# Performance work log

Measured on AMD Instinct MI355X. Metric: run time of the kernel, lower is better.

## Reference

```python
import jax, jax.numpy as jnp
import numpy as np

EPS = 1e-05
TEMP = 0.03


def setup_inputs() -> dict:
    key = jax.random.key(0)
    ks = jax.random.split(key, 5)
    bs, d = 256, 768
    code_vec = jax.random.normal(ks[0], (bs, d), dtype=jnp.float32)
    nl_vec = jax.random.normal(ks[1], (bs, d), dtype=jnp.float32)
    code_aug_vec = jax.random.normal(ks[2], (bs, d), dtype=jnp.float32)
    W1 = jax.random.normal(ks[3], (4 * d, d), dtype=jnp.float32) / np.sqrt(4 * d)
    b1 = jnp.zeros((d,), dtype=jnp.float32)
    W2 = jax.random.normal(ks[4], (d, 1), dtype=jnp.float32) / np.sqrt(d)
    b2 = jnp.zeros((1,), dtype=jnp.float32)
    return {"code_vec": code_vec, "nl_vec": nl_vec, "code_aug_vec": code_aug_vec,
            "W1": W1, "b1": b1, "W2": W2, "b2": b2}


def _pair_logits(nl, code, W1, b1, W2, b2):
    # MLP(cat([nl_i, code_j, nl_i - code_j, nl_i * code_j])) without the 4d concat:
    # split W1 rows into the four 768-blocks.
    d = nl.shape[1]
    Wa, Wb, Wc, Wd = W1[:d], W1[d:2 * d], W1[2 * d:3 * d], W1[3 * d:]
    lin = (nl @ (Wa + Wc))[:, None, :] + (code @ (Wb - Wc))[None, :, :]  # [bs,bs,768]
    prod = jnp.einsum('id,jd,dh->ijh', nl, code, Wd)                      # [bs,bs,768]
    h = jnp.tanh(lin + prod + b1)
    return jax.nn.sigmoid(jnp.einsum('ijh,ho->ij', h, W2) + b2[0])        # [bs,bs]


def _masked_softmax_loss(logits, mask):
    # -log((softmax(logits) * mask).sum(1))
    p = jax.nn.softmax(logits, axis=1)
    return -jnp.log((p * mask).sum(1))


def reference(code_vec, nl_vec, code_aug_vec, W1, b1, W2, b2):
    bs = code_vec.shape[0]
    eye = jnp.eye(bs, dtype=code_vec.dtype)

    # CE over dot-product scores with diagonal labels
    scores = nl_vec @ code_vec.T
    loss_ce = -jnp.mean(jnp.diagonal(jax.nn.log_softmax(scores, axis=1)))

    # Pairwise concat-MLP binary loss
    logits = _pair_logits(nl_vec, code_vec, W1, b1, W2, b2)
    poss = jnp.diagonal(logits)
    neg_log = jnp.log(1.0 - logits + EPS) * (1.0 - eye)
    negs_mean = neg_log.sum() / (bs * (bs - 1))
    loss_cls = -(negs_mean + jnp.mean(jnp.log(poss + EPS)))

    # InfoNCE-style multi-term contrastive loss
    cf = code_vec / jnp.linalg.norm(code_vec, axis=1, keepdims=True)
    nf = nl_vec / jnp.linalg.norm(nl_vec, axis=1, keepdims=True)
    af = code_aug_vec / jnp.linalg.norm(code_aug_vec, axis=1, keepdims=True)

    l_code_p = (cf @ nf.T) / TEMP
    l_nl_p = (nf @ cf.T) / TEMP
    l_code_n = ((cf @ cf.T) / TEMP) * (1.0 - eye)
    l_nl_n = ((nf @ nf.T) / TEMP) * (1.0 - eye)
    l_code_pa = (cf @ af.T) / TEMP
    l_nl_pa = (nf @ af.T) / TEMP

    code_logits = jnp.concatenate([l_code_p, 0.8 * l_code_n, 0.1 * l_code_pa], axis=1)
    nl_logits = jnp.concatenate([l_nl_p, 0.8 * l_nl_n, 0.1 * l_nl_pa], axis=1)
    zeros = jnp.zeros((bs, bs), dtype=code_vec.dtype)
    mask = jnp.concatenate([eye, zeros, eye], axis=1)

    loss_code = _masked_softmax_loss(code_logits, mask)
    loss_nl = _masked_softmax_loss(nl_logits, mask)
    loss_clr = (loss_code.mean() + loss_nl.mean()) / 2.0

    loss = loss_ce + 0.1 * loss_clr + loss_cls
    return (loss, code_vec, nl_vec)
```

## Files before the change

kernel.cpp:

```cpp
#include <hip/hip_runtime.h>
#include <stdint.h>

#define EPSV 1e-5f
#define INVT (1.0f/0.03f)

typedef _Float16 halfx8 __attribute__((ext_vector_type(8)));
typedef float f32x4 __attribute__((ext_vector_type(4)));

__device__ __forceinline__ unsigned short f2h(float f) {
  _Float16 h = (_Float16)f;
  return __builtin_bit_cast(unsigned short, h);
}

__device__ __forceinline__ float wave_sum(float v) {
  #pragma unroll
  for (int m = 32; m; m >>= 1) v += __shfl_xor(v, m);
  return v;
}
__device__ __forceinline__ float wave_max(float v) {
  #pragma unroll
  for (int m = 32; m; m >>= 1) v = fmaxf(v, __shfl_xor(v, m));
  return v;
}
__device__ __forceinline__ float block_sum(float v, float* sred) {
  v = wave_sum(v);
  __syncthreads();
  if ((threadIdx.x & 63) == 0) sred[threadIdx.x >> 6] = v;
  __syncthreads();
  return sred[0] + sred[1] + sred[2] + sred[3];
}
__device__ __forceinline__ float block_max(float v, float* sred) {
  v = wave_max(v);
  __syncthreads();
  if ((threadIdx.x & 63) == 0) sred[threadIdx.x >> 6] = v;
  __syncthreads();
  return fmaxf(fmaxf(sred[0], sred[1]), fmaxf(sred[2], sred[3]));
}

__device__ __forceinline__ void gload_lds16(const void* g, void* l) {
  __builtin_amdgcn_global_load_lds((__attribute__((address_space(1))) void*)g,
                                   (__attribute__((address_space(3))) void*)l, 16, 0, 0);
}

__global__ __launch_bounds__(256) void k_prep(
    const float* __restrict__ code, const float* __restrict__ nl, const float* __restrict__ aug,
    const float* __restrict__ W1,
    unsigned short* __restrict__ code_f16, unsigned short* __restrict__ nl_f16,
    unsigned short* __restrict__ WdT, unsigned short* __restrict__ WbcT,
    unsigned short* __restrict__ lin1_f16,
    float* __restrict__ invc, float* __restrict__ invn, float* __restrict__ inva,
    float* __restrict__ G,
    float* __restrict__ out, float* __restrict__ s_sum, float* __restrict__ accv) {
  __shared__ __align__(16) float smem[4112];
  const int b = blockIdx.x, tid = threadIdx.x;

  if (b < 96) {
    const int rt = b / 12, ct = b % 12;
    const int r0 = rt * 32, c0 = ct * 64;
    float* Xs = smem;
    float* Ws = smem + 1056;
    const int tx = tid & 15, ty = tid >> 4;
    float a[2][4] = {};
    for (int kt = 0; kt < 24; ++kt) {
      const int k0 = kt * 32;
      __syncthreads();
      #pragma unroll
      for (int q = 0; q < 4; ++q) {
        int e = q * 256 + tid;
        int row = e >> 5, k = e & 31;
        Xs[row * 33 + k] = nl[(r0 + row) * 768 + k0 + k];
      }
      #pragma unroll
      for (int q = 0; q < 8; ++q) {
        int e = q * 256 + tid;
        int k = e >> 6, c = e & 63;
        Ws[k * 64 + c] = W1[(k0 + k) * 768 + c0 + c] + W1[(1536 + k0 + k) * 768 + c0 + c];
      }
      __syncthreads();
      #pragma unroll
      for (int k = 0; k < 32; ++k) {
        float xa = Xs[ty * 33 + k], xb = Xs[(ty + 16) * 33 + k];
        float w0 = Ws[k * 64 + tx], w1 = Ws[k * 64 + tx + 16];
        float w2 = Ws[k * 64 + tx + 32], w3 = Ws[k * 64 + tx + 48];
        a[0][0] += xa * w0; a[0][1] += xa * w1; a[0][2] += xa * w2; a[0][3] += xa * w3;
        a[1][0] += xb * w0; a[1][1] += xb * w1; a[1][2] += xb * w2; a[1][3] += xb * w3;
      }
    }
    #pragma unroll
    for (int dy = 0; dy < 2; ++dy)
      #pragma unroll
      for (int m = 0; m < 4; ++m)
        lin1_f16[(r0 + ty + dy * 16) * 768 + c0 + tx + m * 16] = f2h(a[dy][m]);

  } else if (b < 416) {
    const int bb = b - 96;
    const int mat = bb >> 6;
    const int tile = bb & 63;
    const int y0 = (tile >> 3) * 32, x0 = (tile & 7) * 32;
    const float* X; const float* Y;
    if (mat == 0)      { X = nl;   Y = code; }
    else if (mat == 1) { X = code; Y = code; }
    else if (mat == 2) { X = nl;   Y = nl;   }
    else if (mat == 3) { X = code; Y = aug;  }
    else               { X = nl;   Y = aug;  }
    float* outg = G + mat * 65536;
    float* Xs = smem;
    float* Ys = smem + 2048;
    const int tx = tid & 15, ty = tid >> 4;
    float a00 = 0, a01 = 0, a10 = 0, a11 = 0;
    for (int kt = 0; kt < 12; ++kt) {
      const int k0 = kt * 64;
      __syncthreads();
      #pragma unroll
      for (int q = 0; q < 2; ++q) {
        int chunk = q * 256 + tid;
        int row = chunk >> 4, c4 = chunk & 15;
        float4 xv = *(const float4*)(X + (y0 + row) * 768 + k0 + c4 * 4);
        float4 yv = *(const float4*)(Y + (x0 + row) * 768 + k0 + c4 * 4);
        *(float4*)(Xs + row * 64 + ((c4 ^ (row & 15)) << 2)) = xv;
        *(float4*)(Ys + row * 64 + ((c4 ^ (row & 15)) << 2)) = yv;
      }
      __syncthreads();
      #pragma unroll
      for (int c4 = 0; c4 < 16; ++c4) {
        float4 xa = *(const float4*)(Xs + ty * 64 + ((c4 ^ ty) << 2));
        float4 xb = *(const float4*)(Xs + (ty + 16) * 64 + ((c4 ^ ty) << 2));
        float4 ya = *(const float4*)(Ys + tx * 64 + ((c4 ^ tx) << 2));
        float4 yb = *(const float4*)(Ys + (tx + 16) * 64 + ((c4 ^ tx) << 2));
        a00 += xa.x * ya.x + xa.y * ya.y + xa.z * ya.z + xa.w * ya.w;
        a01 += xa.x * yb.x + xa.y * yb.y + xa.z * yb.z + xa.w * yb.w;
        a10 += xb.x * ya.x + xb.y * ya.y + xb.z * ya.z + xb.w * ya.w;
        a11 += xb.x * yb.x + xb.y * yb.y + xb.z * yb.z + xb.w * yb.w;
      }
    }
    outg[(y0 + ty) * 256 + x0 + tx] = a00;
    outg[(y0 + ty) * 256 + x0 + tx + 16] = a01;
    outg[(y0 + ty + 16) * 256 + x0 + tx] = a10;
    outg[(y0 + ty + 16) * 256 + x0 + tx + 16] = a11;

  } else if (b < 800) {
    const int idx = (b - 416) * 256 + tid;
    if (idx < 49152) {
      float4 v = ((const float4*)code)[idx];
      ushort4 o; o.x = f2h(v.x); o.y = f2h(v.y); o.z = f2h(v.z); o.w = f2h(v.w);
      ((ushort4*)code_f16)[idx] = o;
    } else {
      const int q = idx - 49152;
      float4 v = ((const float4*)nl)[q];
      ushort4 o; o.x = f2h(v.x); o.y = f2h(v.y); o.z = f2h(v.z); o.w = f2h(v.w);
      ((ushort4*)nl_f16)[q] = o;
    }

  } else if (b < 1376) {
    float (*tile)[33] = (float(*)[33])smem;
    const int bb = b - 800;
    const int bx = bb % 24, by = bb / 24;
    const int tx = tid & 31, ty = tid >> 5;
    const int h0 = bx * 32, d0 = by * 32;
    #pragma unroll
    for (int yy = 0; yy < 4; ++yy) {
      int dd = ty + yy * 8;
      tile[dd][tx] = W1[(2304 + d0 + dd) * 768 + h0 + tx];
    }
    __syncthreads();
    #pragma unroll
    for (int yy = 0; yy < 4; ++yy) {
      int hh = ty + yy * 8;
      WdT[(h0 + hh) * 768 + d0 + tx] = f2h(tile[tx][hh]);
    }

  } else if (b < 1952) {
    float (*tile)[33] = (float(*)[33])smem;
    const int bb = b - 1376;
    const int bx = bb % 24, by = bb / 24;
    const int tx = tid & 31, ty = tid >> 5;
    const int h0 = bx * 32, d0 = by * 32;
    #pragma unroll
    for (int yy = 0; yy < 4; ++yy) {
      int dd = ty + yy * 8;
      tile[dd][tx] = W1[(768 + d0 + dd) * 768 + h0 + tx] - W1[(1536 + d0 + dd) * 768 + h0 + tx];
    }
    __syncthreads();
    #pragma unroll
    for (int yy = 0; yy < 4; ++yy) {
      int hh = ty + yy * 8;
      WbcT[(h0 + hh) * 768 + d0 + tx] = f2h(tile[tx][hh]);
    }

  } else if (b < 2144) {
    const int rr = (b - 1952) * 4 + (tid >> 6);
    const int mat = rr >> 8, row = rr & 255;
    const float* src = (mat == 0) ? code : (mat == 1) ? nl : aug;
    const int l = tid & 63;
    float s = 0.f;
    #pragma unroll
    for (int t = 0; t < 12; ++t) { float v = src[row * 768 + l + t * 64]; s += v * v; }
    s = wave_sum(s);
    if (l == 0) ((mat == 0) ? invc : (mat == 1) ? invn : inva)[row] = rsqrtf(s);

  } else if (b < 2528) {
    const int idx = (b - 2144) * 256 + tid;
    for (int t = idx; t < 196608; t += 384 * 256) {
      out[1 + t] = code[t];
      out[1 + 196608 + t] = nl[t];
    }

  } else {
    const int idx = (b - 2528) * 256 + tid;
    ((float4*)s_sum)[idx] = make_float4(0.f, 0.f, 0.f, 0.f);
    if (b == 2528 && tid < 16) accv[tid] = 0.f;
  }
}

__global__ __launch_bounds__(512, 4) void k_pair(
    const unsigned short* __restrict__ code_f16, const unsigned short* __restrict__ nl_f16,
    const unsigned short* __restrict__ WdT, const unsigned short* __restrict__ WbcT,
    const unsigned short* __restrict__ lin1_f16,
    const float* __restrict__ b1, const float* __restrict__ W2,
    float* __restrict__ s_sum) {
  __shared__ __align__(16) unsigned short Alds[256 * 64];
  __shared__ __align__(16) unsigned short Blds[128 * 64];
  __shared__ float linb[128];
  __shared__ float w2s[128];
  __shared__ float part[2][256];

  const int tid = threadIdx.x;
  const int bid = blockIdx.x;
  const int ct = bid >> 8;
  const int i  = bid & 255;
  const int h0 = ct << 7;

  if (tid < 128) {
    linb[tid] = (float)((const _Float16*)lin1_f16)[i * 768 + h0 + tid] + b1[h0 + tid];
    w2s[tid]  = W2[h0 + tid];
  }

  const int w = tid >> 6, lane = tid & 63;
  const int lr = lane & 15, g = lane >> 4;
  const int wr = (w >> 1) << 6;
  const int wcIdx = w & 1;
  const int wc = wcIdx << 6;
  const int c4 = tid & 7, rg = tid >> 3;

  f32x4 acc[4][4] = {};

  auto stage_A = [&](int kt) {
    const int k0 = kt << 6;
    #pragma unroll
    for (int q = 0; q < 4; ++q) {
      const int chunk = q * 512 + tid;
      const int row = chunk >> 3, c = chunk & 7;
      const unsigned short* src = code_f16 + row * 768 + k0 + ((c ^ (row & 7)) << 3);
      char* dst = (char*)Alds + (q * 512 + w * 64) * 16;
      gload_lds16(src, dst);
    }
  };

  auto stageB = [&](int kt) {
    const int k0 = kt << 6;
    const uint4 nv  = *(const uint4*)(nl_f16 + i * 768 + k0 + (c4 << 3));
    const uint4 wv0 = *(const uint4*)(WdT  + (h0 + rg) * 768 + k0 + (c4 << 3));
    const uint4 bv0 = *(const uint4*)(WbcT + (h0 + rg) * 768 + k0 + (c4 << 3));
    const uint4 wv1 = *(const uint4*)(WdT  + (h0 + rg + 64) * 768 + k0 + (c4 << 3));
    const uint4 bv1 = *(const uint4*)(WbcT + (h0 + rg + 64) * 768 + k0 + (c4 << 3));
    uint4 p0, p1;
    asm("v_pk_fma_f16 %0, %1, %2, %3" : "=v"(p0.x) : "v"(nv.x), "v"(wv0.x), "v"(bv0.x));
    asm("v_pk_fma_f16 %0, %1, %2, %3" : "=v"(p0.y) : "v"(nv.y), "v"(wv0.y), "v"(bv0.y));
    asm("v_pk_fma_f16 %0, %1, %2, %3" : "=v"(p0.z) : "v"(nv.z), "v"(wv0.z), "v"(bv0.z));
    asm("v_pk_fma_f16 %0, %1, %2, %3" : "=v"(p0.w) : "v"(nv.w), "v"(wv0.w), "v"(bv0.w));
    asm("v_pk_fma_f16 %0, %1, %2, %3" : "=v"(p1.x) : "v"(nv.x), "v"(wv1.x), "v"(bv1.x));
    asm("v_pk_fma_f16 %0, %1, %2, %3" : "=v"(p1.y) : "v"(nv.y), "v"(wv1.y), "v"(bv1.y));
    asm("v_pk_fma_f16 %0, %1, %2, %3" : "=v"(p1.z) : "v"(nv.z), "v"(wv1.z), "v"(bv1.z));
    asm("v_pk_fma_f16 %0, %1, %2, %3" : "=v"(p1.w) : "v"(nv.w), "v"(wv1.w), "v"(bv1.w));
    const int r0 = rg, r1 = rg + 64;
    *(uint4*)((char*)Blds + r0 * 128 + ((c4 ^ (r0 & 7)) << 4)) = p0;
    *(uint4*)((char*)Blds + r1 * 128 + ((c4 ^ (r1 & 7)) << 4)) = p1;
  };

  for (int kt = 0; kt < 12; ++kt) {
    if (kt) __syncthreads();
    stage_A(kt);
    stageB(kt);
    __syncthreads();
    #pragma unroll
    for (int ks = 0; ks < 2; ++ks) {
      halfx8 bf[4];
      #pragma unroll
      for (int n = 0; n < 4; ++n) {
        const int row = wc + n * 16 + lr;
        bf[n] = *(const halfx8*)((const char*)Blds + row * 128 + (((ks * 4 + g) ^ (row & 7)) << 4));
      }
      #pragma unroll
      for (int m = 0; m < 4; ++m) {
        const int row = wr + m * 16 + lr;
        halfx8 af = *(const halfx8*)((const char*)Alds + row * 128 + (((ks * 4 + g) ^ (row & 7)) << 4));
        #pragma unroll
        for (int n = 0; n < 4; ++n)
          acc[m][n] = __builtin_amdgcn_mfma_f32_16x16x32_f16(af, bf[n], acc[m][n], 0, 0, 0);
      }
    }
  }

  #pragma unroll
  for (int m = 0; m < 4; ++m) {
    #pragma unroll
    for (int reg = 0; reg < 4; ++reg) {
      const int rloc = wr + m * 16 + g * 4 + reg;
      float rs = 0.f;
      #pragma unroll
      for (int n = 0; n < 4; ++n) {
        const int cc = wc + n * 16 + lr;
        float x = acc[m][n][reg] + linb[cc];
        x = fminf(fmaxf(x, -15.f), 15.f);
        const float e = __expf(2.f * x);
        rs += __fdividef(e - 1.f, e + 1.f) * w2s[cc];
      }
      rs += __shfl_xor(rs, 1); rs += __shfl_xor(rs, 2);
      rs += __shfl_xor(rs, 4); rs += __shfl_xor(rs, 8);
      if (lr == 0) part[wcIdx][rloc] = rs;
    }
  }
  __syncthreads();
  if (tid < 256) atomicAdd(&s_sum[i * 256 + tid], part[0][tid] + part[1][tid]);
}

__global__ __launch_bounds__(256) void k_loss(const float* __restrict__ G,
    const float* __restrict__ invc, const float* __restrict__ invn, const float* __restrict__ inva,
    const float* __restrict__ s_sum, const float* __restrict__ b2, float* __restrict__ acc) {
  __shared__ float sred[4];
  __shared__ float dvals[3];
  const int t = threadIdx.x;
  if (blockIdx.x < 256) {
    const int i = blockIdx.x;
    const float* Snc = G;
    const float* Scc = G + 65536;
    const float* Snn = G + 131072;
    const float* Sca = G + 196608;
    const float* Sna = G + 262144;
    const float ici = invc[i], ini = invn[i];
    const float ict = invc[t], intt = invn[t], iat = inva[t];
    const float snc_it = Snc[i * 256 + t];
    const float snc_ti = Snc[t * 256 + i];
    const float e1 = snc_ti * ici * intt * INVT;
    const float e2 = (t == i) ? 0.f : 0.8f * INVT * Scc[i * 256 + t] * ici * ict;
    const float e3 = 0.1f * INVT * Sca[i * 256 + t] * ici * iat;
    const float f1 = snc_it * ini * ict * INVT;
    const float f2 = (t == i) ? 0.f : 0.8f * INVT * Snn[i * 256 + t] * ini * intt;
    const float f3 = 0.1f * INVT * Sna[i * 256 + t] * ini * iat;

    const float Mce = block_max(snc_it, sred);
    const float Mco = block_max(fmaxf(fmaxf(e1, e2), e3), sred);
    const float Mnl = block_max(fmaxf(fmaxf(f1, f2), f3), sred);
    const float Sce = block_sum(expf(snc_it - Mce), sred);
    const float Sco = block_sum(expf(e1 - Mco) + expf(e2 - Mco) + expf(e3 - Mco), sred);
    const float Snl = block_sum(expf(f1 - Mnl) + expf(f2 - Mnl) + expf(f3 - Mnl), sred);
    if (t == i) {
      dvals[0] = snc_it;
      dvals[1] = expf(e1 - Mco) + expf(e3 - Mco);
      dvals[2] = expf(f1 - Mnl) + expf(f3 - Mnl);
    }
    __syncthreads();
    if (t == 0) {
      atomicAdd(&acc[0], Mce + logf(Sce) - dvals[0]);
      atomicAdd(&acc[1], logf(Sco) - logf(dvals[1]));
      atomicAdd(&acc[2], logf(Snl) - logf(dvals[2]));
    }
  } else {
    const int r = (blockIdx.x - 256) * 256 + t;
    const int i = r >> 8, j = r & 255;
    const float s = s_sum[r] + b2[0];
    const float logit = 1.f / (1.f + expf(-s));
    const float pos = (i == j) ? logf(logit + EPSV) : 0.f;
    const float neg = (i == j) ? 0.f : logf(1.f - logit + EPSV);
    const float ps = block_sum(pos, sred);
    const float ns = block_sum(neg, sred);
    if (t == 0) { atomicAdd(&acc[3], ps); atomicAdd(&acc[4], ns); }
  }
}

__global__ void k_final(const float* __restrict__ acc, float* __restrict__ out) {
  if (threadIdx.x == 0 && blockIdx.x == 0) {
    const float lce = acc[0] * (1.f / 256.f);
    const float lclr = (acc[1] * (1.f / 256.f) + acc[2] * (1.f / 256.f)) * 0.5f;
    const float lcls = -(acc[4] * (1.f / (256.f * 255.f)) + acc[3] * (1.f / 256.f));
    out[0] = lce + 0.1f * lclr + lcls;
  }
}

extern "C" void kernel_launch(void* const* d_in, const int* in_sizes, int n_in,
                              void* d_out, int out_size, void* d_ws, size_t ws_size,
                              hipStream_t stream) {
  const float* code = (const float*)d_in[0];
  const float* nl   = (const float*)d_in[1];
  const float* aug  = (const float*)d_in[2];
  const float* W1   = (const float*)d_in[3];
  const float* b1   = (const float*)d_in[4];
  const float* W2   = (const float*)d_in[5];
  const float* b2   = (const float*)d_in[6];
  float* out = (float*)d_out;
  char* ws = (char*)d_ws;

  unsigned short* WdT      = (unsigned short*)(ws + 0);
  unsigned short* WbcT     = (unsigned short*)(ws + 1179648);
  unsigned short* code_f16 = (unsigned short*)(ws + 2359296);
  unsigned short* nl_f16   = (unsigned short*)(ws + 2752512);
  unsigned short* lin1_f16 = (unsigned short*)(ws + 3145728);
  float* G    = (float*)(ws + 3538944);
  float* invc = (float*)(ws + 4849664);
  float* invn = (float*)(ws + 4850688);
  float* inva = (float*)(ws + 4851712);
  float* s_sum = (float*)(ws + 4852736);
  float* acc   = (float*)(ws + 5114880);

  k_prep<<<2592, 256, 0, stream>>>(code, nl, aug, W1, code_f16, nl_f16, WdT, WbcT,
                                   lin1_f16, invc, invn, inva, G, out, s_sum, acc);
  k_pair<<<1536, 512, 0, stream>>>(code_f16, nl_f16, WdT, WbcT, lin1_f16, b1, W2, s_sum);
  k_loss<<<512, 256, 0, stream>>>(G, invc, invn, inva, s_sum, b2, acc);
  k_final<<<1, 1, 0, stream>>>(acc, out);
}
```

Baseline: 238.2 us.

## Retile pair kernel to two nl rows by 128 code rows per block

Each pair-MLP block now covers two nl indices and half of the code rows (128) instead of one nl index over all 256 code rows. The A tile (code) is halved and shared by both nl rows, and each block builds two B tiles that reuse the same Wd/Wbc loads. This halves the A-tile global-to-LDS traffic per unit of work and amortizes weight loads across two rows. In exchange, the per-block B-tile build work doubles, and wave-to-tile mapping and the atomic output indexing change.

```diff
diff --git a/kernel.cpp b/kernel.cpp
--- a/kernel.cpp
+++ b/kernel.cpp
@@ -218,27 +218,34 @@
     const unsigned short* __restrict__ lin1_f16,
     const float* __restrict__ b1, const float* __restrict__ W2,
     float* __restrict__ s_sum) {
-  __shared__ __align__(16) unsigned short Alds[256 * 64];
-  __shared__ __align__(16) unsigned short Blds[128 * 64];
-  __shared__ float linb[128];
+  __shared__ __align__(16) unsigned short Alds[128 * 64];
+  __shared__ __align__(16) unsigned short Blds[2][128 * 64];
+  __shared__ float linb[2][128];
   __shared__ float w2s[128];
-  __shared__ float part[2][256];
+  __shared__ float part[2][2][128];
 
   const int tid = threadIdx.x;
   const int bid = blockIdx.x;
   const int ct = bid >> 8;
-  const int i  = bid & 255;
+  const int r  = bid & 255;
+  const int jt = r >> 7;
+  const int ip = r & 127;
+  const int i0 = ip << 1;
   const int h0 = ct << 7;
-
-  if (tid < 128) {
-    linb[tid] = (float)((const _Float16*)lin1_f16)[i * 768 + h0 + tid] + b1[h0 + tid];
-    w2s[tid]  = W2[h0 + tid];
-  }
+  const int j0 = jt << 7;
+
+  if (tid < 256) {
+    const int ihh = tid >> 7, hh = tid & 127;
+    linb[ihh][hh] = (float)((const _Float16*)lin1_f16)[(i0 + ihh) * 768 + h0 + hh] + b1[h0 + hh];
+  }
+  if (tid < 128) w2s[tid] = W2[h0 + tid];
 
   const int w = tid >> 6, lane = tid & 63;
   const int lr = lane & 15, g = lane >> 4;
-  const int wr = (w >> 1) << 6;
-  const int wcIdx = w & 1;
+  const int ih = w >> 2;
+  const int wq = w & 3;
+  const int wr = (wq >> 1) << 6;
+  const int wcIdx = wq & 1;
   const int wc = wcIdx << 6;
   const int c4 = tid & 7, rg = tid >> 3;
 
@@ -247,10 +254,10 @@
   auto stage_A = [&](int kt) {
     const int k0 = kt << 6;
     #pragma unroll
-    for (int q = 0; q < 4; ++q) {
+    for (int q = 0; q < 2; ++q) {
       const int chunk = q * 512 + tid;
       const int row = chunk >> 3, c = chunk & 7;
-      const unsigned short* src = code_f16 + row * 768 + k0 + ((c ^ (row & 7)) << 3);
+      const unsigned short* src = code_f16 + (j0 + row) * 768 + k0 + ((c ^ (row & 7)) << 3);
       char* dst = (char*)Alds + (q * 512 + w * 64) * 16;
       gload_lds16(src, dst);
     }
@@ -258,24 +265,44 @@
 
   auto stageB = [&](int kt) {
     const int k0 = kt << 6;
-    const uint4 nv  = *(const uint4*)(nl_f16 + i * 768 + k0 + (c4 << 3));
-    const uint4 wv0 = *(const uint4*)(WdT  + (h0 + rg) * 768 + k0 + (c4 << 3));
-    const uint4 bv0 = *(const uint4*)(WbcT + (h0 + rg) * 768 + k0 + (c4 << 3));
-    const uint4 wv1 = *(const uint4*)(WdT  + (h0 + rg + 64) * 768 + k0 + (c4 << 3));
-    const uint4 bv1 = *(const uint4*)(WbcT + (h0 + rg + 64) * 768 + k0 + (c4 << 3));
-    uint4 p0, p1;
-    asm("v_pk_fma_f16 %0, %1, %2, %3" : "=v"(p0.x) : "v"(nv.x), "v"(wv0.x), "v"(bv0.x));
-    asm("v_pk_fma_f16 %0, %1, %2, %3" : "=v"(p0.y) : "v"(nv.y), "v"(wv0.y), "v"(bv0.y));
-    asm("v_pk_fma_f16 %0, %1, %2, %3" : "=v"(p0.z) : "v"(nv.z), "v"(wv0.z), "v"(bv0.z));
-    asm("v_pk_fma_f16 %0, %1, %2, %3" : "=v"(p0.w) : "v"(nv.w), "v"(wv0.w), "v"(bv0.w));
-    asm("v_pk_fma_f16 %0, %1, %2, %3" : "=v"(p1.x) : "v"(nv.x), "v"(wv1.x), "v"(bv1.x));
-    asm("v_pk_fma_f16 %0, %1, %2, %3" : "=v"(p1.y) : "v"(nv.y), "v"(wv1.y), "v"(bv1.y));
-    asm("v_pk_fma_f16 %0, %1, %2, %3" : "=v"(p1.z) : "v"(nv.z), "v"(wv1.z), "v"(bv1.z));
-    asm("v_pk_fma_f16 %0, %1, %2, %3" : "=v"(p1.w) : "v"(nv.w), "v"(wv1.w), "v"(bv1.w));
-    const int r0 = rg, r1 = rg + 64;
-    *(uint4*)((char*)Blds + r0 * 128 + ((c4 ^ (r0 & 7)) << 4)) = p0;
-    *(uint4*)((char*)Blds + r1 * 128 + ((c4 ^ (r1 & 7)) << 4)) = p1;
+    const unsigned short* wp = WdT  + (h0 + rg) * 768 + k0 + (c4 << 3);
+    const unsigned short* bp = WbcT + (h0 + rg) * 768 + k0 + (c4 << 3);
+    const uint4 wv0 = *(const uint4*)wp;
+    const uint4 bv0 = *(const uint4*)bp;
+    const uint4 wv1 = *(const uint4*)(wp + 64 * 768);
+    const uint4 bv1 = *(const uint4*)(bp + 64 * 768);
+    const uint4 nv0 = *(const uint4*)(nl_f16 + i0 * 768 + k0 + (c4 << 3));
+    const int sw = (c4 ^ (rg & 7)) << 4;
+    {
+      uint4 p0, p1;
+      asm("v_pk_fma_f16 %0, %1, %2, %3" : "=v"(p0.x) : "v"(nv0.x), "v"(wv0.x), "v"(bv0.x));
+      asm("v_pk_fma_f16 %0, %1, %2, %3" : "=v"(p0.y) : "v"(nv0.y), "v"(wv0.y), "v"(bv0.y));
+      asm("v_pk_fma_f16 %0, %1, %2, %3" : "=v"(p0.z) : "v"(nv0.z), "v"(wv0.z), "v"(bv0.z));
+      asm("v_pk_fma_f16 %0, %1, %2, %3" : "=v"(p0.w) : "v"(nv0.w), "v"(wv0.w), "v"(bv0.w));
+      asm("v_pk_fma_f16 %0, %1, %2, %3" : "=v"(p1.x) : "v"(nv0.x), "v"(wv1.x), "v"(bv1.x));
+      asm("v_pk_fma_f16 %0, %1, %2, %3" : "=v"(p1.y) : "v"(nv0.y), "v"(wv1.y), "v"(bv1.y));
+      asm("v_pk_fma_f16 %0, %1, %2, %3" : "=v"(p1.z) : "v"(nv0.z), "v"(wv1.z), "v"(bv1.z));
+      asm("v_pk_fma_f16 %0, %1, %2, %3" : "=v"(p1.w) : "v"(nv0.w), "v"(wv1.w), "v"(bv1.w));
+      *(uint4*)((char*)&Blds[0][0] + rg * 128 + sw) = p0;
+      *(uint4*)((char*)&Blds[0][0] + (rg + 64) * 128 + sw) = p1;
+    }
+    const uint4 nv1 = *(const uint4*)(nl_f16 + (i0 + 1) * 768 + k0 + (c4 << 3));
+    {
+      uint4 p0, p1;
+      asm("v_pk_fma_f16 %0, %1, %2, %3" : "=v"(p0.x) : "v"(nv1.x), "v"(wv0.x), "v"(bv0.x));
+      asm("v_pk_fma_f16 %0, %1, %2, %3" : "=v"(p0.y) : "v"(nv1.y), "v"(wv0.y), "v"(bv0.y));
+      asm("v_pk_fma_f16 %0, %1, %2, %3" : "=v"(p0.z) : "v"(nv1.z), "v"(wv0.z), "v"(bv0.z));
+      asm("v_pk_fma_f16 %0, %1, %2, %3" : "=v"(p0.w) : "v"(nv1.w), "v"(wv0.w), "v"(bv0.w));
+      asm("v_pk_fma_f16 %0, %1, %2, %3" : "=v"(p1.x) : "v"(nv1.x), "v"(wv1.x), "v"(bv1.x));
+      asm("v_pk_fma_f16 %0, %1, %2, %3" : "=v"(p1.y) : "v"(nv1.y), "v"(wv1.y), "v"(bv1.y));
+      asm("v_pk_fma_f16 %0, %1, %2, %3" : "=v"(p1.z) : "v"(nv1.z), "v"(wv1.z), "v"(bv1.z));
+      asm("v_pk_fma_f16 %0, %1, %2, %3" : "=v"(p1.w) : "v"(nv1.w), "v"(wv1.w), "v"(bv1.w));
+      *(uint4*)((char*)&Blds[1][0] + rg * 128 + sw) = p0;
+      *(uint4*)((char*)&Blds[1][0] + (rg + 64) * 128 + sw) = p1;
+    }
   };
+
+  const unsigned short* Bbase = &Blds[ih][0];
 
   for (int kt = 0; kt < 12; ++kt) {
     if (kt) __syncthreads();
@@ -288,7 +315,7 @@
       #pragma unroll
       for (int n = 0; n < 4; ++n) {
         const int row = wc + n * 16 + lr;
-        bf[n] = *(const halfx8*)((const char*)Blds + row * 128 + (((ks * 4 + g) ^ (row & 7)) << 4));
+        bf[n] = *(const halfx8*)((const char*)Bbase + row * 128 + (((ks * 4 + g) ^ (row & 7)) << 4));
       }
       #pragma unroll
       for (int m = 0; m < 4; ++m) {
@@ -305,23 +332,26 @@
   for (int m = 0; m < 4; ++m) {
     #pragma unroll
     for (int reg = 0; reg < 4; ++reg) {
-      const int rloc = wr + m * 16 + g * 4 + reg;
+      const int jloc = wr + m * 16 + g * 4 + reg;
       float rs = 0.f;
       #pragma unroll
       for (int n = 0; n < 4; ++n) {
         const int cc = wc + n * 16 + lr;
-        float x = acc[m][n][reg] + linb[cc];
+        float x = acc[m][n][reg] + linb[ih][cc];
         x = fminf(fmaxf(x, -15.f), 15.f);
         const float e = __expf(2.f * x);
         rs += __fdividef(e - 1.f, e + 1.f) * w2s[cc];
       }
       rs += __shfl_xor(rs, 1); rs += __shfl_xor(rs, 2);
       rs += __shfl_xor(rs, 4); rs += __shfl_xor(rs, 8);
-      if (lr == 0) part[wcIdx][rloc] = rs;
+      if (lr == 0) part[ih][wcIdx][jloc] = rs;
     }
   }
   __syncthreads();
-  if (tid < 256) atomicAdd(&s_sum[i * 256 + tid], part[0][tid] + part[1][tid]);
+  if (tid < 256) {
+    const int ihh = tid >> 7, jj = tid & 127;
+    atomicAdd(&s_sum[(i0 + ihh) * 256 + j0 + jj], part[ihh][0][jj] + part[ihh][1][jj]);
+  }
 }
 
 __global__ __launch_bounds__(256) void k_loss(const float* __restrict__ G,
```

After: 229.6 us. 3.6% less time.
